# Optimization experiments

Measured on AMD Instinct MI355X. Metric: run time of the kernel, lower is better.

## Reference

```python
import jax, jax.numpy as jnp
import numpy as np

WINDOW_SIZE = 20
NEG_BIG = -1e8  # matches -10**8 in the torch mask


def band_mask(S):
    # 0 inside the sliding window |i-j| <= WINDOW_SIZE, -1e8 outside (additive mask)
    idx = jnp.arange(S)
    return jnp.where(jnp.abs(idx[:, None] - idx[None, :]) <= WINDOW_SIZE, 0.0, NEG_BIG).astype(jnp.float32)


def setup_inputs() -> dict:
    key = jax.random.key(0)
    k1, k2, k3, k4 = jax.random.split(key, 4)
    B, S, Dq, Dk = 8, 2048, 1024, 1024
    queries = jax.random.normal(k1, (B, S, Dq), dtype=jnp.float32)
    keys = jax.random.normal(k2, (B, S, Dk), dtype=jnp.float32)
    # reduce = nn.Linear(key_dim, query_dim) since key_dim >= query_dim
    lim = 1.0 / np.sqrt(Dk)
    W_reduce = jax.random.uniform(k3, (Dq, Dk), jnp.float32, -lim, lim)
    b_reduce = jax.random.uniform(k4, (Dq,), jnp.float32, -lim, lim)
    return {"queries": queries, "keys": keys, "W_reduce": W_reduce, "b_reduce": b_reduce}


def reference(queries, keys, W_reduce, b_reduce):
    # values default to the ORIGINAL keys (before dim matching)
    values = keys
    # match_dims: reduce keys to query_dim
    keys_r = jnp.einsum('bkd,qd->bkq', keys, W_reduce) + b_reduce  # [B,S,Dq]
    sims = jnp.einsum('bqd,bkd->bqk', queries, keys_r)             # [B,S,S]
    sims = sims + band_mask(queries.shape[1])                      # additive banded window mask
    weights = jax.nn.softmax(sims, axis=-1)
    return jnp.einsum('bqk,bkd->bqd', weights, values)
```

## Files before the change

### kernel.cpp

```cpp
#include <hip/hip_runtime.h>


#define BATCH 8
#define SEQ   2048
#define DIM   1024
#define WIN   20

typedef _Float16 half8  __attribute__((ext_vector_type(8)));
typedef _Float16 half4v __attribute__((ext_vector_type(4)));
typedef float    f32x4  __attribute__((ext_vector_type(4)));

#define GLOAD_LDS16(gsrc, ldst)                                                        \
    __builtin_amdgcn_global_load_lds(                                                  \
        (const __attribute__((address_space(1))) void*)(gsrc),                         \
        (__attribute__((address_space(3))) void*)(ldst), 16, 0, 0)

__global__ __launch_bounds__(256) void cvt_q_f16(const float* __restrict__ in,
                                                 _Float16* __restrict__ out) {
    const int n8 = (BATCH * SEQ * DIM) / 8;
    for (int i = blockIdx.x * 256 + threadIdx.x; i < n8; i += gridDim.x * 256) {
        const float4 a = ((const float4*)in)[2 * i];
        const float4 b = ((const float4*)in)[2 * i + 1];
        half8 h;
        h[0] = (_Float16)a.x; h[1] = (_Float16)a.y; h[2] = (_Float16)a.z; h[3] = (_Float16)a.w;
        h[4] = (_Float16)b.x; h[5] = (_Float16)b.y; h[6] = (_Float16)b.z; h[7] = (_Float16)b.w;
        ((half8*)out)[i] = h;
    }
}

#define WTS 68
__global__ __launch_bounds__(256) void cvt_w_t(const float* __restrict__ W,
                                               _Float16* __restrict__ WT) {
    __shared__ _Float16 tile[64 * WTS];
    const int k0 = blockIdx.x * 64;
    const int n0 = blockIdx.y * 64;
    const int t  = threadIdx.x;
    const int r  = t >> 4;
    const int c4 = (t & 15) * 4;
    #pragma unroll
    for (int rr = 0; rr < 64; rr += 16) {
        float4 v = *(const float4*)&W[(size_t)(k0 + rr + r) * DIM + n0 + c4];
        _Float16* dst = &tile[(rr + r) * WTS + c4];
        dst[0] = (_Float16)v.x; dst[1] = (_Float16)v.y;
        dst[2] = (_Float16)v.z; dst[3] = (_Float16)v.w;
    }
    __syncthreads();
    #pragma unroll
    for (int rr = 0; rr < 64; rr += 16) {
        const int n = rr + r;
        half4v h = { tile[(c4 + 0) * WTS + n], tile[(c4 + 1) * WTS + n],
                     tile[(c4 + 2) * WTS + n], tile[(c4 + 3) * WTS + n] };
        *(half4v*)&WT[(size_t)(n0 + n) * DIM + k0 + c4] = h;
    }
}

#define GK 64
__global__ __launch_bounds__(256, 2) void gemm_f16t(const _Float16* __restrict__ A,
                                                    const _Float16* __restrict__ B,
                                                    _Float16* __restrict__ C) {
    __shared__ _Float16 As[128 * GK];
    __shared__ _Float16 Bs[128 * GK];

    const int m0   = blockIdx.x * 128;
    const int n0   = blockIdx.y * 128;
    const int t    = threadIdx.x;
    const int lane = t & 63;
    const int wv   = t >> 6;
    const int wm   = (wv >> 1) * 64;
    const int wn   = (wv & 1) * 64;
    const int l15  = lane & 15;
    const int quad = lane >> 4;

    const int srow = lane >> 3;
    const int sck  = (lane & 7) ^ srow;

    f32x4 acc[4][4] = {};

    for (int k0 = 0; k0 < DIM; k0 += GK) {
        __syncthreads();
        #pragma unroll
        for (int j = 0; j < 4; ++j) {
            const int rs = (j * 4 + wv) * 8;
            GLOAD_LDS16(A + (size_t)(m0 + rs + srow) * DIM + k0 + sck * 8, &As[rs * GK]);
            GLOAD_LDS16(B + (size_t)(n0 + rs + srow) * DIM + k0 + sck * 8, &Bs[rs * GK]);
        }
        __syncthreads();

        #pragma unroll
        for (int s = 0; s < 2; ++s) {
            half8 af[4], bf[4];
            #pragma unroll
            for (int i = 0; i < 4; ++i)
                af[i] = *(const half8*)&As[(wm + i * 16 + l15) * GK +
                                           (((s * 4 + quad) ^ (l15 & 7)) * 8)];
            #pragma unroll
            for (int j = 0; j < 4; ++j)
                bf[j] = *(const half8*)&Bs[(wn + j * 16 + l15) * GK +
                                           (((s * 4 + quad) ^ (l15 & 7)) * 8)];
            #pragma unroll
            for (int i = 0; i < 4; ++i)
                #pragma unroll
                for (int j = 0; j < 4; ++j)
                    acc[i][j] = __builtin_amdgcn_mfma_f32_16x16x32_f16(af[i], bf[j], acc[i][j], 0, 0, 0);
        }
    }

    #pragma unroll
    for (int i = 0; i < 4; ++i) {
        #pragma unroll
        for (int r = 0; r < 4; ++r) {
            _Float16* crow = C + (size_t)(m0 + wm + i * 16 + quad * 4 + r) * DIM + n0 + wn + l15;
            #pragma unroll
            for (int j = 0; j < 4; ++j)
                crow[j * 16] = (_Float16)acc[i][j][r];
        }
    }
}

#define LDK 40
__global__ __launch_bounds__(256) void gemm_qw_f16(const float* __restrict__ Q,
                                                   const float* __restrict__ W,
                                                   float* __restrict__ QT) {
    __shared__ _Float16 Asl[128 * LDK];
    __shared__ _Float16 Bsl[128 * LDK];

    const int m0 = blockIdx.x * 128;
    const int n0 = blockIdx.y * 128;
    const int t  = threadIdx.x;
    const int lane = t & 63;
    const int wv   = t >> 6;
    const int wm   = (wv >> 1) * 64;
    const int wn   = (wv & 1) * 64;
    const int l15  = lane & 15;
    const int quad = lane >> 4;

    const int ar = t >> 1;
    const int ac = (t & 1) * 16;
    const float* Aptr = Q + (size_t)(m0 + ar) * DIM + ac;
    _Float16* AsW = &Asl[ar * LDK + ac];

    const int br = t >> 3;
    const int bc = t & 7;
    const float* Bptr = W + (size_t)br * DIM + n0 + bc;

    f32x4 acc[4][4] = {};

    for (int k0 = 0; k0 < DIM; k0 += 32) {
        float4 a0 = *(const float4*)(Aptr + k0);
        float4 a1 = *(const float4*)(Aptr + k0 + 4);
        float4 a2 = *(const float4*)(Aptr + k0 + 8);
        float4 a3 = *(const float4*)(Aptr + k0 + 12);
        float bv[16];
        #pragma unroll
        for (int j = 0; j < 16; ++j) bv[j] = Bptr[(size_t)k0 * DIM + 8 * j];

        __syncthreads();

        half8 h0, h1;
        h0[0] = (_Float16)a0.x; h0[1] = (_Float16)a0.y; h0[2] = (_Float16)a0.z; h0[3] = (_Float16)a0.w;
        h0[4] = (_Float16)a1.x; h0[5] = (_Float16)a1.y; h0[6] = (_Float16)a1.z; h0[7] = (_Float16)a1.w;
        h1[0] = (_Float16)a2.x; h1[1] = (_Float16)a2.y; h1[2] = (_Float16)a2.z; h1[3] = (_Float16)a2.w;
        h1[4] = (_Float16)a3.x; h1[5] = (_Float16)a3.y; h1[6] = (_Float16)a3.z; h1[7] = (_Float16)a3.w;
        *(half8*)(AsW)     = h0;
        *(half8*)(AsW + 8) = h1;

        #pragma unroll
        for (int j = 0; j < 16; ++j)
            Bsl[(bc + 8 * j) * LDK + br] = (_Float16)bv[j];

        __syncthreads();

        half8 af[4], bf[4];
        #pragma unroll
        for (int i = 0; i < 4; ++i)
            af[i] = *(const half8*)&Asl[(wm + i * 16 + l15) * LDK + quad * 8];
        #pragma unroll
        for (int j = 0; j < 4; ++j)
            bf[j] = *(const half8*)&Bsl[(wn + j * 16 + l15) * LDK + quad * 8];

        #pragma unroll
        for (int i = 0; i < 4; ++i)
            #pragma unroll
            for (int j = 0; j < 4; ++j)
                acc[i][j] = __builtin_amdgcn_mfma_f32_16x16x32_f16(af[i], bf[j], acc[i][j], 0, 0, 0);
    }

    #pragma unroll
    for (int i = 0; i < 4; ++i) {
        const int row0 = m0 + wm + i * 16 + quad * 4;
        #pragma unroll
        for (int r = 0; r < 4; ++r) {
            float* orow = QT + (size_t)(row0 + r) * DIM + n0 + wn + l15;
            #pragma unroll
            for (int j = 0; j < 4; ++j)
                orow[j * 16] = acc[i][j][r];
        }
    }
}

#define TQ  16
#define KP  64
#define KLD 80
#define QLD 80
#define SLD 66

template <typename QTT>
__global__ __launch_bounds__(256, 4) void attn_mfma(const QTT* __restrict__ QT,
                                                    const float* __restrict__ Keys,
                                                    float* __restrict__ Out) {
    const int blk  = blockIdx.x;
    const int b    = blk & 7;
    const int tile = blk >> 3;
    const int q0   = tile * TQ;
    const int t    = threadIdx.x;
    const int lane = t & 63;
    const int wv   = t >> 6;
    const int l15  = lane & 15;
    const int quad = lane >> 4;

    const int klo = (q0 - WIN) > 0 ? (q0 - WIN) : 0;
    const int khi = (q0 + TQ - 1 + WIN) < (SEQ - 1) ? (q0 + TQ - 1 + WIN) : (SEQ - 1);
    const int nk  = khi - klo + 1;

    const QTT*   qt   = QT + ((size_t)b * SEQ + q0) * DIM;
    const float* keys = Keys + (size_t)b * SEQ * DIM;

    __shared__ _Float16 Qc[TQ * QLD];
    __shared__ _Float16 Ks[KP * KLD];
    __shared__ float    Sl[TQ * SLD];
    __shared__ float    Wl[TQ * SLD];

    const int qr = t >> 4;
    const int qc = (t & 15) * 4;
    const int kr = t >> 2;
    const int kc = (t & 3) * 4;
    const int krow = (klo + kr) < (SEQ - 1) ? (klo + kr) : (SEQ - 1);

    const QTT*   qsrc = qt + (size_t)qr * DIM + qc;
    const float* ksrc = keys + (size_t)krow * DIM + kc;

    f32x4 acc_s = {};

    for (int d0 = 0; d0 < DIM; d0 += 64) {
        half4v hq;
        if constexpr (sizeof(QTT) == 2) {
            hq = *(const half4v*)(qsrc + d0);
        } else {
            const float4 qv = *(const float4*)(qsrc + d0);
            hq = half4v{(_Float16)qv.x, (_Float16)qv.y, (_Float16)qv.z, (_Float16)qv.w};
        }
        float4 kv0 = *(const float4*)(ksrc + d0);
        float4 kv1 = *(const float4*)(ksrc + d0 + 16);
        float4 kv2 = *(const float4*)(ksrc + d0 + 32);
        float4 kv3 = *(const float4*)(ksrc + d0 + 48);

        __syncthreads();

        *(half4v*)&Qc[qr * QLD + qc] = hq;
        half4v h0 = {(_Float16)kv0.x, (_Float16)kv0.y, (_Float16)kv0.z, (_Float16)kv0.w};
        half4v h1 = {(_Float16)kv1.x, (_Float16)kv1.y, (_Float16)kv1.z, (_Float16)kv1.w};
        half4v h2 = {(_Float16)kv2.x, (_Float16)kv2.y, (_Float16)kv2.z, (_Float16)kv2.w};
        half4v h3 = {(_Float16)kv3.x, (_Float16)kv3.y, (_Float16)kv3.z, (_Float16)kv3.w};
        *(half4v*)&Ks[kr * KLD + kc]      = h0;
        *(half4v*)&Ks[kr * KLD + kc + 16] = h1;
        *(half4v*)&Ks[kr * KLD + kc + 32] = h2;
        *(half4v*)&Ks[kr * KLD + kc + 48] = h3;

        __syncthreads();

        #pragma unroll
        for (int s = 0; s < 2; ++s) {
            half8 af = *(const half8*)&Qc[l15 * QLD + s * 32 + quad * 8];
            half8 bf = *(const half8*)&Ks[(wv * 16 + l15) * KLD + s * 32 + quad * 8];
            acc_s = __builtin_amdgcn_mfma_f32_16x16x32_f16(af, bf, acc_s, 0, 0, 0);
        }
    }

    __syncthreads();
    #pragma unroll
    for (int r = 0; r < 4; ++r) {
        const int q = quad * 4 + r;
        const int c = wv * 16 + l15;
        const int d = (q0 + q) - (klo + c);
        const bool valid = (c < nk) && ((unsigned)(d + WIN) <= 2u * WIN);
        Sl[q * SLD + c] = valid ? acc_s[r] : -1e30f;
    }
    __syncthreads();

    if (t < 64) {
        const int q = t >> 2, part = t & 3;
        const float* srow = &Sl[q * SLD + part * 16];
        float*       wrow = &Wl[q * SLD + part * 16];
        float m = -1e30f;
        #pragma unroll
        for (int i = 0; i < 16; ++i) m = fmaxf(m, srow[i]);
        m = fmaxf(m, __shfl_xor(m, 1));
        m = fmaxf(m, __shfl_xor(m, 2));
        float ssum = 0.f;
        #pragma unroll
        for (int i = 0; i < 16; ++i) { float e = expf(srow[i] - m); wrow[i] = e; ssum += e; }
        ssum += __shfl_xor(ssum, 1);
        ssum += __shfl_xor(ssum, 2);
        const float inv = 1.f / ssum;
        #pragma unroll
        for (int i = 0; i < 16; ++i) wrow[i] *= inv;
    }
    __syncthreads();

    float accs[TQ][4] = {};
    for (int c = 0; c < nk; ++c) {
        const float* krow2 = keys + (size_t)(klo + c) * DIM;
        const float k0 = krow2[t], k1 = krow2[t + 256], k2 = krow2[t + 512], k3 = krow2[t + 768];
        #pragma unroll
        for (int q = 0; q < TQ; ++q) {
            const float w = Wl[q * SLD + c];
            accs[q][0] = fmaf(w, k0, accs[q][0]);
            accs[q][1] = fmaf(w, k1, accs[q][1]);
            accs[q][2] = fmaf(w, k2, accs[q][2]);
            accs[q][3] = fmaf(w, k3, accs[q][3]);
        }
    }
    #pragma unroll
    for (int q = 0; q < TQ; ++q) {
        float* orow = Out + ((size_t)b * SEQ + q0 + q) * DIM;
        orow[t]       = accs[q][0];
        orow[t + 256] = accs[q][1];
        orow[t + 512] = accs[q][2];
        orow[t + 768] = accs[q][3];
    }
}

extern "C" void kernel_launch(void* const* d_in, const int* in_sizes, int n_in,
                              void* d_out, int out_size, void* d_ws, size_t ws_size,
                              hipStream_t stream) {
    const float* queries = (const float*)d_in[0];
    const float* keys    = (const float*)d_in[1];
    const float* W       = (const float*)d_in[2];
    float* out = (float*)d_out;

    const size_t qt16_bytes = (size_t)BATCH * SEQ * DIM * sizeof(_Float16);
    const size_t w16_bytes  = (size_t)DIM * DIM * sizeof(_Float16);
    const int nblk = (BATCH * SEQ) / TQ;

    if (ws_size >= qt16_bytes + w16_bytes) {
        _Float16* q16  = (_Float16*)d_out;
        _Float16* qt16 = (_Float16*)d_ws;
        _Float16* w16t = (_Float16*)((char*)d_ws + qt16_bytes);

        cvt_q_f16<<<2048, 256, 0, stream>>>(queries, q16);
        cvt_w_t<<<dim3(16, 16), 256, 0, stream>>>(W, w16t);
        gemm_f16t<<<dim3(128, 8), 256, 0, stream>>>(q16, w16t, qt16);
        attn_mfma<_Float16><<<nblk, 256, 0, stream>>>(qt16, keys, out);
    } else {
        gemm_qw_f16<<<dim3(128, 8), 256, 0, stream>>>(queries, W, out);
        attn_mfma<float><<<nblk, 256, 0, stream>>>(out, keys, out);
    }
}
```

Baseline: 256.9 us.

## Load attention score operands directly into MFMA registers, skip LDS staging

Adds a new attention kernel that computes the QK scores by loading the f16 query rows and fp32 key rows straight from global memory into MFMA fragments. This removes the per-step LDS staging and the two barriers per 64-wide chunk. The weighted-sum stage now uses float4 key loads and processes the queries in two halves of 8 to cut register use. The GEMM grid is also swapped so consecutive blocks walk along N and reuse the same A rows. Direct global fragment loads are less coalesced (32-byte strided per lane), which may raise memory traffic in exchange for fewer synchronisations.

After: 298.8 us. +16.3%, slower.

```diff
diff --git a/kernel.cpp b/kernel.cpp
--- a/kernel.cpp
+++ b/kernel.cpp
@@ -61,8 +61,8 @@
     __shared__ _Float16 As[128 * GK];
     __shared__ _Float16 Bs[128 * GK];
 
-    const int m0   = blockIdx.x * 128;
-    const int n0   = blockIdx.y * 128;
+    const int m0   = blockIdx.y * 128;
+    const int n0   = blockIdx.x * 128;
     const int t    = threadIdx.x;
     const int lane = t & 63;
     const int wv   = t >> 6;
@@ -114,6 +114,101 @@
             for (int j = 0; j < 4; ++j)
                 crow[j * 16] = (_Float16)acc[i][j][r];
         }
+    }
+}
+
+#define TQ  16
+#define SLD 66
+
+__global__ __launch_bounds__(256) void attn_v3(const _Float16* __restrict__ QT,
+                                               const float* __restrict__ Keys,
+                                               float* __restrict__ Out) {
+    const int blk  = blockIdx.x;
+    const int b    = blk & 7;
+    const int tile = blk >> 3;
+    const int q0   = tile * TQ;
+    const int t    = threadIdx.x;
+    const int lane = t & 63;
+    const int wv   = t >> 6;
+    const int l15  = lane & 15;
+    const int quad = lane >> 4;
+
+    const int klo = (q0 - WIN) > 0 ? (q0 - WIN) : 0;
+    const int khi = (q0 + TQ - 1 + WIN) < (SEQ - 1) ? (q0 + TQ - 1 + WIN) : (SEQ - 1);
+    const int nk  = khi - klo + 1;
+
+    const float* keys = Keys + (size_t)b * SEQ * DIM;
+
+    __shared__ float Sl[TQ * SLD];
+    __shared__ float Wl[TQ * SLD];
+
+    const _Float16* qrow = QT + ((size_t)b * SEQ + q0 + l15) * DIM + quad * 8;
+    int kcol = klo + wv * 16 + l15;
+    if (kcol > SEQ - 1) kcol = SEQ - 1;
+    const float* krow = keys + (size_t)kcol * DIM + quad * 8;
+
+    f32x4 acc_s = {};
+    #pragma unroll 4
+    for (int dk = 0; dk < DIM; dk += 32) {
+        half8 af = *(const half8*)(qrow + dk);
+        float4 b0 = *(const float4*)(krow + dk);
+        float4 b1 = *(const float4*)(krow + dk + 4);
+        half8 bf;
+        bf[0] = (_Float16)b0.x; bf[1] = (_Float16)b0.y;
+        bf[2] = (_Float16)b0.z; bf[3] = (_Float16)b0.w;
+        bf[4] = (_Float16)b1.x; bf[5] = (_Float16)b1.y;
+        bf[6] = (_Float16)b1.z; bf[7] = (_Float16)b1.w;
+        acc_s = __builtin_amdgcn_mfma_f32_16x16x32_f16(af, bf, acc_s, 0, 0, 0);
+    }
+
+    #pragma unroll
+    for (int r = 0; r < 4; ++r) {
+        const int q = quad * 4 + r;
+        const int c = wv * 16 + l15;
+        const int d = (q0 + q) - (klo + c);
+        const bool valid = (c < nk) && ((unsigned)(d + WIN) <= 2u * WIN);
+        Sl[q * SLD + c] = valid ? acc_s[r] : -1e30f;
+    }
+    __syncthreads();
+
+    if (t < 64) {
+        const int q = t >> 2, part = t & 3;
+        const float* srow = &Sl[q * SLD + part * 16];
+        float*       wrow = &Wl[q * SLD + part * 16];
+        float m = -1e30f;
+        #pragma unroll
+        for (int i = 0; i < 16; ++i) m = fmaxf(m, srow[i]);
+        m = fmaxf(m, __shfl_xor(m, 1));
+        m = fmaxf(m, __shfl_xor(m, 2));
+        float ssum = 0.f;
+        #pragma unroll
+        for (int i = 0; i < 16; ++i) { float e = expf(srow[i] - m); wrow[i] = e; ssum += e; }
+        ssum += __shfl_xor(ssum, 1);
+        ssum += __shfl_xor(ssum, 2);
+        const float inv = 1.f / ssum;
+        #pragma unroll
+        for (int i = 0; i < 16; ++i) wrow[i] *= inv;
+    }
+    __syncthreads();
+
+    const int d4 = t * 4;
+    #pragma unroll
+    for (int qh = 0; qh < 2; ++qh) {
+        float4 accs[8] = {};
+        for (int c = 0; c < nk; ++c) {
+            const float4 kv = *(const float4*)(keys + (size_t)(klo + c) * DIM + d4);
+            #pragma unroll
+            for (int q = 0; q < 8; ++q) {
+                const float w = Wl[(qh * 8 + q) * SLD + c];
+                accs[q].x = fmaf(w, kv.x, accs[q].x);
+                accs[q].y = fmaf(w, kv.y, accs[q].y);
+                accs[q].z = fmaf(w, kv.z, accs[q].z);
+                accs[q].w = fmaf(w, kv.w, accs[q].w);
+            }
+        }
+        #pragma unroll
+        for (int q = 0; q < 8; ++q)
+            *(float4*)(Out + ((size_t)b * SEQ + q0 + qh * 8 + q) * DIM + d4) = accs[q];
     }
 }
 
@@ -198,16 +293,13 @@
     }
 }
 
-#define TQ  16
 #define KP  64
 #define KLD 80
 #define QLD 80
-#define SLD 66
-
-template <typename QTT>
-__global__ __launch_bounds__(256, 4) void attn_mfma(const QTT* __restrict__ QT,
-                                                    const float* __restrict__ Keys,
-                                                    float* __restrict__ Out) {
+
+__global__ __launch_bounds__(256, 4) void attn_fb(const float* __restrict__ QT,
+                                                  const float* __restrict__ Keys,
+                                                  float* __restrict__ Out) {
     const int blk  = blockIdx.x;
     const int b    = blk & 7;
     const int tile = blk >> 3;
@@ -222,7 +314,7 @@
     const int khi = (q0 + TQ - 1 + WIN) < (SEQ - 1) ? (q0 + TQ - 1 + WIN) : (SEQ - 1);
     const int nk  = khi - klo + 1;
 
-    const QTT*   qt   = QT + ((size_t)b * SEQ + q0) * DIM;
+    const float* qt   = QT + ((size_t)b * SEQ + q0) * DIM;
     const float* keys = Keys + (size_t)b * SEQ * DIM;
 
     __shared__ _Float16 Qc[TQ * QLD];
@@ -236,19 +328,13 @@
     const int kc = (t & 3) * 4;
     const int krow = (klo + kr) < (SEQ - 1) ? (klo + kr) : (SEQ - 1);
 
-    const QTT*   qsrc = qt + (size_t)qr * DIM + qc;
+    const float* qsrc = qt + (size_t)qr * DIM + qc;
     const float* ksrc = keys + (size_t)krow * DIM + kc;
 
     f32x4 acc_s = {};
 
     for (int d0 = 0; d0 < DIM; d0 += 64) {
-        half4v hq;
-        if constexpr (sizeof(QTT) == 2) {
-            hq = *(const half4v*)(qsrc + d0);
-        } else {
-            const float4 qv = *(const float4*)(qsrc + d0);
-            hq = half4v{(_Float16)qv.x, (_Float16)qv.y, (_Float16)qv.z, (_Float16)qv.w};
-        }
+        const float4 qv = *(const float4*)(qsrc + d0);
         float4 kv0 = *(const float4*)(ksrc + d0);
         float4 kv1 = *(const float4*)(ksrc + d0 + 16);
         float4 kv2 = *(const float4*)(ksrc + d0 + 32);
@@ -256,6 +342,7 @@
 
         __syncthreads();
 
+        half4v hq = {(_Float16)qv.x, (_Float16)qv.y, (_Float16)qv.z, (_Float16)qv.w};
         *(half4v*)&Qc[qr * QLD + qc] = hq;
         half4v h0 = {(_Float16)kv0.x, (_Float16)kv0.y, (_Float16)kv0.z, (_Float16)kv0.w};
         half4v h1 = {(_Float16)kv1.x, (_Float16)kv1.y, (_Float16)kv1.z, (_Float16)kv1.w};
@@ -307,26 +394,24 @@
     }
     __syncthreads();
 
-    float accs[TQ][4] = {};
-    for (int c = 0; c < nk; ++c) {
-        const float* krow2 = keys + (size_t)(klo + c) * DIM;
-        const float k0 = krow2[t], k1 = krow2[t + 256], k2 = krow2[t + 512], k3 = krow2[t + 768];
-        #pragma unroll
-        for (int q = 0; q < TQ; ++q) {
-            const float w = Wl[q * SLD + c];
-            accs[q][0] = fmaf(w, k0, accs[q][0]);
-            accs[q][1] = fmaf(w, k1, accs[q][1]);
-            accs[q][2] = fmaf(w, k2, accs[q][2]);
-            accs[q][3] = fmaf(w, k3, accs[q][3]);
-        }
-    }
-    #pragma unroll
-    for (int q = 0; q < TQ; ++q) {
-        float* orow = Out + ((size_t)b * SEQ + q0 + q) * DIM;
-        orow[t]       = accs[q][0];
-        orow[t + 256] = accs[q][1];
-        orow[t + 512] = accs[q][2];
-        orow[t + 768] = accs[q][3];
+    const int d4 = t * 4;
+    #pragma unroll
+    for (int qh = 0; qh < 2; ++qh) {
+        float4 accs[8] = {};
+        for (int c = 0; c < nk; ++c) {
+            const float4 kv = *(const float4*)(keys + (size_t)(klo + c) * DIM + d4);
+            #pragma unroll
+            for (int q = 0; q < 8; ++q) {
+                const float w = Wl[(qh * 8 + q) * SLD + c];
+                accs[q].x = fmaf(w, kv.x, accs[q].x);
+                accs[q].y = fmaf(w, kv.y, accs[q].y);
+                accs[q].z = fmaf(w, kv.z, accs[q].z);
+                accs[q].w = fmaf(w, kv.w, accs[q].w);
+            }
+        }
+        #pragma unroll
+        for (int q = 0; q < 8; ++q)
+            *(float4*)(Out + ((size_t)b * SEQ + q0 + qh * 8 + q) * DIM + d4) = accs[q];
     }
 }
 
@@ -349,10 +434,10 @@
 
         cvt_q_f16<<<2048, 256, 0, stream>>>(queries, q16);
         cvt_w_t<<<dim3(16, 16), 256, 0, stream>>>(W, w16t);
-        gemm_f16t<<<dim3(128, 8), 256, 0, stream>>>(q16, w16t, qt16);
-        attn_mfma<_Float16><<<nblk, 256, 0, stream>>>(qt16, keys, out);
+        gemm_f16t<<<dim3(8, 128), 256, 0, stream>>>(q16, w16t, qt16);
+        attn_v3<<<nblk, 256, 0, stream>>>(qt16, keys, out);
     } else {
         gemm_qw_f16<<<dim3(128, 8), 256, 0, stream>>>(queries, W, out);
-        attn_mfma<float><<<nblk, 256, 0, stream>>>(out, keys, out);
-    }
-}
+        attn_fb<<<nblk, 256, 0, stream>>>(out, keys, out);
+    }
+}
```

## Add 32-query-tile attention kernel with 512 threads and swap GEMM grid order

Applied to the files above, without the earlier changes.

Replaces the 16-query attention kernel on the fast path with a new kernel that processes 32 queries per block using 8 waves. The key window of up to 72 rows is loaded once for twice as many queries, so each key row is read and converted fewer times across neighbouring tiles. The GEMM grid is also transposed so consecutive blocks share the same M rows, which changes L2 reuse order. The trade-offs are higher register pressure from 32 float2 accumulators and uneven MFMA work across waves, since wave 0 of each group handles the extra 16-key tile.

Result: slower. 279.0 us (+8.6%).

```diff
diff --git a/kernel.cpp b/kernel.cpp
--- a/kernel.cpp
+++ b/kernel.cpp
@@ -61,8 +61,8 @@
     __shared__ _Float16 As[128 * GK];
     __shared__ _Float16 Bs[128 * GK];
 
-    const int m0   = blockIdx.x * 128;
-    const int n0   = blockIdx.y * 128;
+    const int m0   = blockIdx.y * 128;
+    const int n0   = blockIdx.x * 128;
     const int t    = threadIdx.x;
     const int lane = t & 63;
     const int wv   = t >> 6;
@@ -117,6 +117,167 @@
     }
 }
 
+#define TQV  32
+#define KPV  80
+#define KLD2 80
+#define QLD2 80
+#define SLD2 84
+
+__global__ __launch_bounds__(512, 4) void attn_v4(const _Float16* __restrict__ QT,
+                                                  const float* __restrict__ Keys,
+                                                  float* __restrict__ Out) {
+    const int blk  = blockIdx.x;
+    const int b    = blk & 7;
+    const int tile = blk >> 3;
+    const int q0   = tile * TQV;
+    const int t    = threadIdx.x;
+    const int lane = t & 63;
+    const int wv   = t >> 6;
+    const int l15  = lane & 15;
+    const int quad = lane >> 4;
+
+    const int klo = (q0 - WIN) > 0 ? (q0 - WIN) : 0;
+    const int khi = (q0 + TQV - 1 + WIN) < (SEQ - 1) ? (q0 + TQV - 1 + WIN) : (SEQ - 1);
+    const int nk  = khi - klo + 1;
+
+    const float* keys = Keys + (size_t)b * SEQ * DIM;
+
+    __shared__ _Float16 Qc[TQV * QLD2];
+    __shared__ _Float16 Ks[KPV * KLD2];
+    __shared__ float    Sl[TQV * SLD2];
+    __shared__ float    Wl[TQV * SLD2];
+
+    const int qr = t >> 4;
+    const int qc = (t & 15) * 4;
+    const int kr = t >> 3;
+    const int kc = (t & 7) * 8;
+    const int krow0 = (klo + kr) < (SEQ - 1) ? (klo + kr) : (SEQ - 1);
+    const int kr2   = 64 + (t >> 3);
+    const int krow2 = (klo + kr2) < (SEQ - 1) ? (klo + kr2) : (SEQ - 1);
+
+    const _Float16* qsrc = QT + ((size_t)b * SEQ + q0 + qr) * DIM + qc;
+    const float*    ksrc0 = keys + (size_t)krow0 * DIM + kc;
+    const float*    ksrc2 = keys + (size_t)krow2 * DIM + kc;
+
+    const int qt_w = wv >> 2;
+    const int kt_a = wv & 3;
+    const bool two = (kt_a == 0);
+
+    f32x4 acc0 = {}, acc1 = {};
+
+    for (int d0 = 0; d0 < DIM; d0 += 64) {
+        half4v hq = *(const half4v*)(qsrc + d0);
+        float4 kv0 = *(const float4*)(ksrc0 + d0);
+        float4 kv1 = *(const float4*)(ksrc0 + d0 + 4);
+        float4 kv2, kv3;
+        if (t < 128) {
+            kv2 = *(const float4*)(ksrc2 + d0);
+            kv3 = *(const float4*)(ksrc2 + d0 + 4);
+        }
+
+        __syncthreads();
+
+        *(half4v*)&Qc[qr * QLD2 + qc] = hq;
+        half8 h0;
+        h0[0] = (_Float16)kv0.x; h0[1] = (_Float16)kv0.y;
+        h0[2] = (_Float16)kv0.z; h0[3] = (_Float16)kv0.w;
+        h0[4] = (_Float16)kv1.x; h0[5] = (_Float16)kv1.y;
+        h0[6] = (_Float16)kv1.z; h0[7] = (_Float16)kv1.w;
+        *(half8*)&Ks[kr * KLD2 + kc] = h0;
+        if (t < 128) {
+            half8 h2;
+            h2[0] = (_Float16)kv2.x; h2[1] = (_Float16)kv2.y;
+            h2[2] = (_Float16)kv2.z; h2[3] = (_Float16)kv2.w;
+            h2[4] = (_Float16)kv3.x; h2[5] = (_Float16)kv3.y;
+            h2[6] = (_Float16)kv3.z; h2[7] = (_Float16)kv3.w;
+            *(half8*)&Ks[kr2 * KLD2 + kc] = h2;
+        }
+
+        __syncthreads();
+
+        #pragma unroll
+        for (int s = 0; s < 2; ++s) {
+            half8 af = *(const half8*)&Qc[(qt_w * 16 + l15) * QLD2 + s * 32 + quad * 8];
+            half8 bf0 = *(const half8*)&Ks[(kt_a * 16 + l15) * KLD2 + s * 32 + quad * 8];
+            acc0 = __builtin_amdgcn_mfma_f32_16x16x32_f16(af, bf0, acc0, 0, 0, 0);
+            if (two) {
+                half8 bf1 = *(const half8*)&Ks[(4 * 16 + l15) * KLD2 + s * 32 + quad * 8];
+                acc1 = __builtin_amdgcn_mfma_f32_16x16x32_f16(af, bf1, acc1, 0, 0, 0);
+            }
+        }
+    }
+
+    __syncthreads();
+    #pragma unroll
+    for (int r = 0; r < 4; ++r) {
+        const int q = qt_w * 16 + quad * 4 + r;
+        {
+            const int c = kt_a * 16 + l15;
+            const int d = (q0 + q) - (klo + c);
+            const bool valid = (c < nk) && ((unsigned)(d + WIN) <= 2u * WIN);
+            Sl[q * SLD2 + c] = valid ? acc0[r] : -1e30f;
+        }
+        if (two) {
+            const int c = 64 + l15;
+            const int d = (q0 + q) - (klo + c);
+            const bool valid = (c < nk) && ((unsigned)(d + WIN) <= 2u * WIN);
+            Sl[q * SLD2 + c] = valid ? acc1[r] : -1e30f;
+        }
+    }
+    __syncthreads();
+
+    if (t < 128) {
+        const int q = t >> 2, part = t & 3;
+        const float* srow = &Sl[q * SLD2 + part * 20];
+        float*       wrow = &Wl[q * SLD2 + part * 20];
+        float m = -1e30f;
+        #pragma unroll
+        for (int i = 0; i < 20; ++i) m = fmaxf(m, srow[i]);
+        m = fmaxf(m, __shfl_xor(m, 1));
+        m = fmaxf(m, __shfl_xor(m, 2));
+        float ssum = 0.f;
+        #pragma unroll
+        for (int i = 0; i < 20; ++i) { float e = expf(srow[i] - m); wrow[i] = e; ssum += e; }
+        ssum += __shfl_xor(ssum, 1);
+        ssum += __shfl_xor(ssum, 2);
+        const float inv = 1.f / ssum;
+        #pragma unroll
+        for (int i = 0; i < 20; ++i) wrow[i] *= inv;
+    }
+    __syncthreads();
+
+    float2 accs[TQV] = {};
+    int c = 0;
+    for (; c + 1 < nk; c += 2) {
+        const float* ka = keys + (size_t)(klo + c) * DIM;
+        const float* kb = keys + (size_t)(klo + c + 1) * DIM;
+        const float a0 = ka[t], a1 = ka[t + 512];
+        const float b0 = kb[t], b1 = kb[t + 512];
+        #pragma unroll
+        for (int q = 0; q < TQV; ++q) {
+            const float2 w = *(const float2*)&Wl[q * SLD2 + c];
+            accs[q].x = fmaf(w.x, a0, fmaf(w.y, b0, accs[q].x));
+            accs[q].y = fmaf(w.x, a1, fmaf(w.y, b1, accs[q].y));
+        }
+    }
+    if (c < nk) {
+        const float* ka = keys + (size_t)(klo + c) * DIM;
+        const float a0 = ka[t], a1 = ka[t + 512];
+        #pragma unroll
+        for (int q = 0; q < TQV; ++q) {
+            const float w = Wl[q * SLD2 + c];
+            accs[q].x = fmaf(w, a0, accs[q].x);
+            accs[q].y = fmaf(w, a1, accs[q].y);
+        }
+    }
+    #pragma unroll
+    for (int q = 0; q < TQV; ++q) {
+        float* orow = Out + ((size_t)b * SEQ + q0 + q) * DIM;
+        orow[t]       = accs[q].x;
+        orow[t + 512] = accs[q].y;
+    }
+}
+
 #define LDK 40
 __global__ __launch_bounds__(256) void gemm_qw_f16(const float* __restrict__ Q,
                                                    const float* __restrict__ W,
@@ -204,10 +365,9 @@
 #define QLD 80
 #define SLD 66
 
-template <typename QTT>
-__global__ __launch_bounds__(256, 4) void attn_mfma(const QTT* __restrict__ QT,
-                                                    const float* __restrict__ Keys,
-                                                    float* __restrict__ Out) {
+__global__ __launch_bounds__(256, 4) void attn_fb(const float* __restrict__ QT,
+                                                  const float* __restrict__ Keys,
+                                                  float* __restrict__ Out) {
     const int blk  = blockIdx.x;
     const int b    = blk & 7;
     const int tile = blk >> 3;
@@ -222,7 +382,7 @@
     const int khi = (q0 + TQ - 1 + WIN) < (SEQ - 1) ? (q0 + TQ - 1 + WIN) : (SEQ - 1);
     const int nk  = khi - klo + 1;
 
-    const QTT*   qt   = QT + ((size_t)b * SEQ + q0) * DIM;
+    const float* qt   = QT + ((size_t)b * SEQ + q0) * DIM;
     const float* keys = Keys + (size_t)b * SEQ * DIM;
 
     __shared__ _Float16 Qc[TQ * QLD];
@@ -236,19 +396,13 @@
     const int kc = (t & 3) * 4;
     const int krow = (klo + kr) < (SEQ - 1) ? (klo + kr) : (SEQ - 1);
 
-    const QTT*   qsrc = qt + (size_t)qr * DIM + qc;
+    const float* qsrc = qt + (size_t)qr * DIM + qc;
     const float* ksrc = keys + (size_t)krow * DIM + kc;
 
     f32x4 acc_s = {};
 
     for (int d0 = 0; d0 < DIM; d0 += 64) {
-        half4v hq;
-        if constexpr (sizeof(QTT) == 2) {
-            hq = *(const half4v*)(qsrc + d0);
-        } else {
-            const float4 qv = *(const float4*)(qsrc + d0);
-            hq = half4v{(_Float16)qv.x, (_Float16)qv.y, (_Float16)qv.z, (_Float16)qv.w};
-        }
+        const float4 qv = *(const float4*)(qsrc + d0);
         float4 kv0 = *(const float4*)(ksrc + d0);
         float4 kv1 = *(const float4*)(ksrc + d0 + 16);
         float4 kv2 = *(const float4*)(ksrc + d0 + 32);
@@ -256,6 +410,7 @@
 
         __syncthreads();
 
+        half4v hq = {(_Float16)qv.x, (_Float16)qv.y, (_Float16)qv.z, (_Float16)qv.w};
         *(half4v*)&Qc[qr * QLD + qc] = hq;
         half4v h0 = {(_Float16)kv0.x, (_Float16)kv0.y, (_Float16)kv0.z, (_Float16)kv0.w};
         half4v h1 = {(_Float16)kv1.x, (_Float16)kv1.y, (_Float16)kv1.z, (_Float16)kv1.w};
@@ -340,7 +495,6 @@
 
     const size_t qt16_bytes = (size_t)BATCH * SEQ * DIM * sizeof(_Float16);
     const size_t w16_bytes  = (size_t)DIM * DIM * sizeof(_Float16);
-    const int nblk = (BATCH * SEQ) / TQ;
 
     if (ws_size >= qt16_bytes + w16_bytes) {
         _Float16* q16  = (_Float16*)d_out;
@@ -349,10 +503,12 @@
 
         cvt_q_f16<<<2048, 256, 0, stream>>>(queries, q16);
         cvt_w_t<<<dim3(16, 16), 256, 0, stream>>>(W, w16t);
-        gemm_f16t<<<dim3(128, 8), 256, 0, stream>>>(q16, w16t, qt16);
-        attn_mfma<_Float16><<<nblk, 256, 0, stream>>>(qt16, keys, out);
+        gemm_f16t<<<dim3(8, 128), 256, 0, stream>>>(q16, w16t, qt16);
+        const int nblk = (BATCH * SEQ) / TQV;
+        attn_v4<<<nblk, 512, 0, stream>>>(qt16, keys, out);
     } else {
         gemm_qw_f16<<<dim3(128, 8), 256, 0, stream>>>(queries, W, out);
-        attn_mfma<float><<<nblk, 256, 0, stream>>>(out, keys, out);
-    }
-}
+        const int nblk = (BATCH * SEQ) / TQ;
+        attn_fb<<<nblk, 256, 0, stream>>>(out, keys, out);
+    }
+}
```
